# Kernel optimization log

Hardware: AMD Instinct MI355X
Metric: run time of the kernel (lower is better)

Reference implementation:

```python
import jax, jax.numpy as jnp
import numpy as np

ALPHA = 0.2  # LeakyReLU negative slope
NEG = -1e12


def setup_inputs() -> dict:
    key = jax.random.key(0)
    ks = jax.random.split(key, 7)
    B, N, Cin, F, H = 4, 2048, 256, 64, 4
    x = jax.random.normal(ks[0], (B, N, Cin), dtype=jnp.float32)
    adj = jax.random.randint(ks[1], (N, N), 0, 2, dtype=jnp.int32)
    W = jax.random.normal(ks[2], (H, Cin, F), dtype=jnp.float32) * (1.414 / np.sqrt(Cin))
    a1 = jax.random.normal(ks[3], (H, F), dtype=jnp.float32) * 0.1
    a2 = jax.random.normal(ks[4], (H, F), dtype=jnp.float32) * 0.1
    Wl = jax.random.normal(ks[5], (F, H * F), dtype=jnp.float32) * (1.0 / np.sqrt(H * F))
    bl = jax.random.normal(ks[6], (F,), dtype=jnp.float32) * 0.01
    return {"x": x, "adj": adj, "W": W, "a1": a1, "a2": a2, "Wl": Wl, "bl": bl}


def leaky(v):
    return jnp.where(v >= 0, v, ALPHA * v)


def reference(x, adj, W, a1, a2, Wl, bl):
    # Eval mode: dropout is a no-op.
    # h: [B,H,N,F] per-head projected features
    h = jnp.einsum("bnc,hcf->bhnf", x, W)
    # additive attention: e[b,h,i,j] = leaky(h_i . a1 + h_j . a2)
    f1 = jnp.einsum("bhnf,hf->bhn", h, a1)  # source term
    f2 = jnp.einsum("bhnf,hf->bhn", h, a2)  # target term
    e = leaky(f1[:, :, :, None] + f2[:, :, None, :])  # [B,H,N,N]
    e = jnp.where(adj[None, None] > 0, e, NEG)
    # NOTE: original softmaxes over dim=1 of [B,N,N], i.e. the i axis (axis=2 here)
    att = jax.nn.softmax(e, axis=2)
    hp = jnp.einsum("bhij,bhjf->bhif", att, h)  # [B,H,N,F]
    hp = jax.nn.relu(hp)  # concat=True heads
    B, H, N, F = hp.shape
    cat = hp.transpose(0, 2, 1, 3).reshape(B, N, H * F)
    out = leaky(cat @ Wl.T + bl)  # n_heads > 1 -> linear + leakyrelu
    return out
```

## Files before the change

### kernel.cpp

```cpp
#include <hip/hip_runtime.h>
#include <hip/hip_bf16.h>
#include <stdint.h>

typedef __attribute__((ext_vector_type(8))) short short8;
typedef __attribute__((ext_vector_type(4))) float f32x4;
typedef uint32_t u32;
typedef uint16_t u16;
typedef uint8_t u8;

#define LOG2E 1.4426950408889634f


__device__ __forceinline__ u16 f2bf(float f){
  union{float f; u32 u;} x; x.f = f;
  u32 r = x.u + 0x7FFFu + ((x.u >> 16) & 1u);
  return (u16)(r >> 16);
}
__device__ __forceinline__ u32 pkbf(float a, float b){
  __hip_bfloat162 h = __float22bfloat162_rn(float2{a, b});
  union{ __hip_bfloat162 h; u32 u; } cv; cv.h = h;
  return cv.u;
}
__device__ __forceinline__ float bflo(u32 cd){ union{u32 u; float f;} v; v.u = cd << 16; return v.f; }
__device__ __forceinline__ float bfhi(u32 cd){ union{u32 u; float f;} v; v.u = cd & 0xFFFF0000u; return v.f; }

__global__ __launch_bounds__(256) void k_front(const float* __restrict__ x,
      const float* __restrict__ W, const float* __restrict__ a1, const float* __restrict__ a2,
      const int* __restrict__ adj,
      u8* __restrict__ adjb, u16* __restrict__ hT,
      float* __restrict__ Aarr, float* __restrict__ Barr,
      float* __restrict__ Cexp, float* __restrict__ Dexp){
  int bid = blockIdx.x, t = threadIdx.x;

  if (bid >= 512){
    int idx = (bid - 512)*256 + t;
    const int4* ap = (const int4*)(adj + (size_t)idx*8);
    int4 v0 = ap[0], v1 = ap[1];
    u32 byte = (u32)(v0.x > 0)        | ((u32)(v0.y > 0) << 1)
             | ((u32)(v0.z > 0) << 2) | ((u32)(v0.w > 0) << 3)
             | ((u32)(v1.x > 0) << 4) | ((u32)(v1.y > 0) << 5)
             | ((u32)(v1.z > 0) << 6) | ((u32)(v1.w > 0) << 7);
    adjb[idx] = (u8)byte;
    return;
  }
  __shared__ u16 WL[64*264];
  int rt = bid & 127, cb = bid >> 7;
  const float* Wh = W + (size_t)cb*16384;
  #pragma unroll 4
  for (int p = 0; p < 16; p++){
    int idx = p*256 + t;
    float4 wv = ((const float4*)Wh)[idx];
    int off = idx*4; int c = off >> 6, f0 = off & 63;
    int cc = c ^ (((f0 >> 2) & 7) << 3);
    WL[(f0+0)*264 + cc] = f2bf(wv.x);
    WL[(f0+1)*264 + cc] = f2bf(wv.y);
    WL[(f0+2)*264 + cc] = f2bf(wv.z);
    WL[(f0+3)*264 + cc] = f2bf(wv.w);
  }
  __syncthreads();

  int w = t >> 6, l = t & 63;
  int rA = rt*64 + w*16 + (l & 15);
  int kg = (l >> 4) * 8;
  int rowq[4], rswq[4];
  #pragma unroll
  for (int q = 0; q < 4; q++){
    rowq[q] = q*16 + (l & 15);
    rswq[q] = ((rowq[q] >> 2) & 7) << 3;
  }
  f32x4 acc[4] = {};
  const float* xrow = x + (size_t)rA * 256;
  #pragma unroll
  for (int ks = 0; ks < 8; ks++){
    int c = ks*32 + kg;
    float4 xa = *(const float4*)(xrow + c);
    float4 xb = *(const float4*)(xrow + c + 4);
    union{u32 w[4]; short8 v;} A;
    A.w[0] = pkbf(xa.x, xa.y); A.w[1] = pkbf(xa.z, xa.w);
    A.w[2] = pkbf(xb.x, xb.y); A.w[3] = pkbf(xb.z, xb.w);
    #pragma unroll
    for (int q = 0; q < 4; q++){
      short8 Bf = *(const short8*)&WL[rowq[q]*264 + (c ^ rswq[q])];
      acc[q] = __builtin_amdgcn_mfma_f32_16x16x32_bf16(A.v, Bf, acc[q], 0, 0, 0);
    }
  }
  int rb = rt*64 + w*16 + (l >> 4)*4;
  int b = rb >> 11, n = rb & 2047;
  #pragma unroll
  for (int q = 0; q < 4; q++){
    int f = q*16 + (l & 15);
    u32 p0 = pkbf(acc[q][0], acc[q][1]);
    u32 p1 = pkbf(acc[q][2], acc[q][3]);
    u16* dst = hT + ((size_t)(b*4 + cb)*64 + f)*2048 + n;
    *(uint2*)dst = uint2{p0, p1};
  }
  float a1v[4], a2v[4];
  #pragma unroll
  for (int q = 0; q < 4; q++){
    a1v[q] = a1[cb*64 + q*16 + (l & 15)];
    a2v[q] = a2[cb*64 + q*16 + (l & 15)];
  }
  float s1[4], s2[4];
  #pragma unroll
  for (int r = 0; r < 4; r++){
    s1[r] = acc[0][r]*a1v[0] + acc[1][r]*a1v[1] + acc[2][r]*a1v[2] + acc[3][r]*a1v[3];
    s2[r] = acc[0][r]*a2v[0] + acc[1][r]*a2v[1] + acc[2][r]*a2v[2] + acc[3][r]*a2v[3];
  }
  #pragma unroll
  for (int m = 1; m <= 8; m <<= 1){
    #pragma unroll
    for (int r = 0; r < 4; r++){
      s1[r] += __shfl_xor(s1[r], m);
      s2[r] += __shfl_xor(s2[r], m);
    }
  }
  if ((l & 15) == 0){
    #pragma unroll
    for (int r = 0; r < 4; r++){
      int row = rb + r;
      int bb = row >> 11, nn = row & 2047;
      int o = (bb*4 + cb)*2048 + nn;
      float fa = s1[r] * LOG2E;
      Aarr[o] = __builtin_amdgcn_exp2f(fa);
      Barr[o] = __builtin_amdgcn_exp2f(0.2f*fa);
      float fb = s2[r] * LOG2E;
      Cexp[o] = __builtin_amdgcn_exp2f(fb);
      Dexp[o] = __builtin_amdgcn_exp2f(0.2f*fb);
    }
  }
}

__global__ __launch_bounds__(256) void k_colsum(const u32* __restrict__ adjw,
      const float* __restrict__ Aarr, const float* __restrict__ Barr,
      const float* __restrict__ Cexp, const float* __restrict__ Dexp,
      float* __restrict__ partial){
  __shared__ float AL[128*16], BL[128*16];
  __shared__ float red[4][1024];
  int jt = blockIdx.x;
  int is = blockIdx.y;
  int t = threadIdx.x, w = t >> 6, l = t & 63;
  int i0 = is*128;
  for (int k = t; k < 2048; k += 256){
    int bh = k >> 7, ii = k & 127;
    float av = Aarr[bh*2048 + i0 + ii];
    float bv = Barr[bh*2048 + i0 + ii];
    AL[ii*16 + bh] = av;
    BL[ii*16 + bh] = bv;
  }
  int j = jt*64 + l;
  float Cj[16], Dj[16];
  #pragma unroll
  for (int bh = 0; bh < 16; bh++){
    Cj[bh] = Cexp[bh*2048 + j];
    Dj[bh] = Dexp[bh*2048 + j];
  }
  float acc[16] = {};
  __syncthreads();
  int wi = jt*2 + (l >> 5), sh = l & 31;
  const u32* aw = adjw + wi;
  #pragma unroll 2
  for (int ii = w*32; ii < w*32 + 32; ii++){
    u32 m = aw[(size_t)(i0 + ii)*64];
    float bitf = (float)((m >> sh) & 1u);
    const float* ar = &AL[ii*16];
    const float* br = &BL[ii*16];
    #pragma unroll
    for (int q = 0; q < 4; q++){
      float4 a4 = *(const float4*)(ar + q*4);
      float4 b4 = *(const float4*)(br + q*4);
      acc[q*4+0] = fmaf(fmaxf(a4.x*Cj[q*4+0], b4.x*Dj[q*4+0]), bitf, acc[q*4+0]);
      acc[q*4+1] = fmaf(fmaxf(a4.y*Cj[q*4+1], b4.y*Dj[q*4+1]), bitf, acc[q*4+1]);
      acc[q*4+2] = fmaf(fmaxf(a4.z*Cj[q*4+2], b4.z*Dj[q*4+2]), bitf, acc[q*4+2]);
      acc[q*4+3] = fmaf(fmaxf(a4.w*Cj[q*4+3], b4.w*Dj[q*4+3]), bitf, acc[q*4+3]);
    }
  }
  #pragma unroll
  for (int bh = 0; bh < 16; bh++) red[w][bh*64 + l] = acc[bh];
  __syncthreads();
  #pragma unroll
  for (int k = 0; k < 4; k++){
    int e = t*4 + k;
    float s = (red[0][e] + red[1][e]) + (red[2][e] + red[3][e]);
    int bh = e >> 6, jl = e & 63;
    partial[((size_t)is*16 + bh)*2048 + jt*64 + jl] = s;
  }
}

__global__ __launch_bounds__(256) void k_cd(const float* __restrict__ partial,
      const float* __restrict__ Cexp, const float* __restrict__ Dexp,
      u32* __restrict__ CD){
  int t = blockIdx.x*256 + threadIdx.x;
  float s = 0.f;
  #pragma unroll
  for (int is = 0; is < 16; is++) s += partial[(size_t)is*32768 + t];
  float inv = 1.0f / s;
  CD[t] = pkbf(Cexp[t]*inv, Dexp[t]*inv);
}

__global__ __launch_bounds__(256) void k_pv(const u32* __restrict__ adjw, const u16* __restrict__ hT,
      const float* __restrict__ Aarr, const float* __restrict__ Barr,
      const u32* __restrict__ CD, float* __restrict__ part){
  int it = blockIdx.x;
  int bh = blockIdx.y;
  int jh = blockIdx.z;
  int b = bh >> 2, h = bh & 3;
  int t = threadIdx.x;
  int w = t >> 6, l = t & 63;

  __shared__ u16 hTl[64*136];

  int i0 = it*128 + w*32 + (l & 15);
  float Ai0 = Aarr[bh*2048 + i0],      Bi0 = Barr[bh*2048 + i0];
  float Ai1 = Aarr[bh*2048 + i0 + 16], Bi1 = Barr[bh*2048 + i0 + 16];
  const u32* CDr = CD + bh*2048;
  const u16* hTr = hT + (size_t)bh * 64 * 2048;
  int kg = (l >> 4) * 8;
  f32x4 acc[2][4] = {};

  for (int jj = 0; jj < 1024; jj += 128){
    int jc = jh*1024 + jj;
    __syncthreads();
    {
      int f = t >> 2, seg = (t & 3) * 32;
      const u16* src = hTr + (size_t)f*2048 + jc + seg;
      u16* d = hTl + f*136 + seg;
      *(uint4*)(d)      = *(const uint4*)(src);
      *(uint4*)(d + 8)  = *(const uint4*)(src + 8);
      *(uint4*)(d + 16) = *(const uint4*)(src + 16);
      *(uint4*)(d + 24) = *(const uint4*)(src + 24);
    }
    __syncthreads();
    uint4 mw0 = *(const uint4*)(adjw + (size_t)i0*64 + (jc >> 5));
    uint4 mw1 = *(const uint4*)(adjw + (size_t)(i0+16)*64 + (jc >> 5));
    #pragma unroll
    for (int ks = 0; ks < 4; ks++){
      u32 cd[8];
      *(uint4*)(cd)     = *(const uint4*)(CDr + jc + ks*32 + kg);
      *(uint4*)(cd + 4) = *(const uint4*)(CDr + jc + ks*32 + kg + 4);
      u32 w0 = (&mw0.x)[ks] >> kg;
      u32 w1 = (&mw1.x)[ks] >> kg;
      float wv0[8], wv1[8];
      #pragma unroll
      for (int e = 0; e < 8; e++){
        float ca = bflo(cd[e]), db = bfhi(cd[e]);
        float ev0 = fmaxf(Ai0*ca, Bi0*db);
        float ev1 = fmaxf(Ai1*ca, Bi1*db);
        wv0[e] = ((int)(w0 << (31-e)) < 0) ? ev0 : 0.f;
        wv1[e] = ((int)(w1 << (31-e)) < 0) ? ev1 : 0.f;
      }
      union{u32 w[4]; short8 v;} A0, A1;
      A0.w[0] = pkbf(wv0[0], wv0[1]); A0.w[1] = pkbf(wv0[2], wv0[3]);
      A0.w[2] = pkbf(wv0[4], wv0[5]); A0.w[3] = pkbf(wv0[6], wv0[7]);
      A1.w[0] = pkbf(wv1[0], wv1[1]); A1.w[1] = pkbf(wv1[2], wv1[3]);
      A1.w[2] = pkbf(wv1[4], wv1[5]); A1.w[3] = pkbf(wv1[6], wv1[7]);
      #pragma unroll
      for (int q = 0; q < 4; q++){
        short8 Bf = *(const short8*)&hTl[(q*16 + (l & 15))*136 + ks*32 + kg];
        acc[0][q] = __builtin_amdgcn_mfma_f32_16x16x32_bf16(A0.v, Bf, acc[0][q], 0, 0, 0);
        acc[1][q] = __builtin_amdgcn_mfma_f32_16x16x32_bf16(A1.v, Bf, acc[1][q], 0, 0, 0);
      }
    }
  }
  float* pr = part + ((size_t)(jh*4 + b)*2048)*256;
  #pragma unroll
  for (int r = 0; r < 2; r++){
    int nb = it*128 + w*32 + r*16 + (l >> 4)*4;
    #pragma unroll
    for (int q = 0; q < 4; q++){
      int f = h*64 + q*16 + (l & 15);
      #pragma unroll
      for (int rr = 0; rr < 4; rr++){
        pr[(size_t)(nb + rr)*256 + f] = acc[r][q][rr];
      }
    }
  }
}

__global__ __launch_bounds__(256) void k_out(const float* __restrict__ part,
                       const float* __restrict__ Wl, const float* __restrict__ bl,
                       float* __restrict__ out){
  int rt = blockIdx.x;
  int w = threadIdx.x >> 6, l = threadIdx.x & 63;
  int rA = rt*64 + w*16 + (l & 15);
  int b = rA >> 11, n = rA & 2047;
  const float* p0 = part + ((size_t)b*2048 + n)*256;
  const float* p1 = part + ((size_t)(4 + b)*2048 + n)*256;
  int kg = (l >> 4) * 8;
  f32x4 acc[4] = {};
  #pragma unroll
  for (int ks = 0; ks < 8; ks++){
    int c = ks*32 + kg;
    float4 x0 = *(const float4*)(p0 + c);
    float4 x1 = *(const float4*)(p0 + c + 4);
    float4 y0 = *(const float4*)(p1 + c);
    float4 y1 = *(const float4*)(p1 + c + 4);
    float av[8];
    av[0] = fmaxf(x0.x + y0.x, 0.f); av[1] = fmaxf(x0.y + y0.y, 0.f);
    av[2] = fmaxf(x0.z + y0.z, 0.f); av[3] = fmaxf(x0.w + y0.w, 0.f);
    av[4] = fmaxf(x1.x + y1.x, 0.f); av[5] = fmaxf(x1.y + y1.y, 0.f);
    av[6] = fmaxf(x1.z + y1.z, 0.f); av[7] = fmaxf(x1.w + y1.w, 0.f);
    union{u32 w[4]; short8 v;} A;
    A.w[0] = pkbf(av[0], av[1]); A.w[1] = pkbf(av[2], av[3]);
    A.w[2] = pkbf(av[4], av[5]); A.w[3] = pkbf(av[6], av[7]);
    #pragma unroll
    for (int q = 0; q < 4; q++){
      const float* wr = Wl + (size_t)(q*16 + (l & 15))*256 + c;
      float4 u0 = *(const float4*)(wr);
      float4 u1 = *(const float4*)(wr + 4);
      union{u32 w[4]; short8 v;} Bv;
      Bv.w[0] = pkbf(u0.x, u0.y); Bv.w[1] = pkbf(u0.z, u0.w);
      Bv.w[2] = pkbf(u1.x, u1.y); Bv.w[3] = pkbf(u1.z, u1.w);
      acc[q] = __builtin_amdgcn_mfma_f32_16x16x32_bf16(A.v, Bv.v, acc[q], 0, 0, 0);
    }
  }
  int rb = rt*64 + w*16 + (l >> 4)*4;
  #pragma unroll
  for (int q = 0; q < 4; q++){
    int o = q*16 + (l & 15);
    float bv = bl[o];
    #pragma unroll
    for (int r = 0; r < 4; r++){
      float v = acc[q][r] + bv;
      out[(size_t)(rb + r)*64 + o] = fmaxf(v, 0.2f*v);
    }
  }
}

extern "C" void kernel_launch(void* const* d_in, const int* in_sizes, int n_in,
                              void* d_out, int out_size, void* d_ws, size_t ws_size,
                              hipStream_t stream) {
  const float* x  = (const float*)d_in[0];
  const int* adj  = (const int*)d_in[1];
  const float* W  = (const float*)d_in[2];
  const float* a1 = (const float*)d_in[3];
  const float* a2 = (const float*)d_in[4];
  const float* Wl = (const float*)d_in[5];
  const float* bl = (const float*)d_in[6];
  float* out = (float*)d_out;
  char* ws = (char*)d_ws;

  u32* adjw    = (u32*)(ws + 0x0000000);
  u16* hT      = (u16*)(ws + 0x0080000);
  float* part  = (float*)(ws + 0x0480000);
  float* Aarr  = (float*)(ws + 0x1480000);
  float* Barr  = (float*)(ws + 0x14A0000);
  float* Cexp  = (float*)(ws + 0x14C0000);
  float* Dexp  = (float*)(ws + 0x14E0000);
  u32* CD      = (u32*)(ws + 0x1500000);

  k_front<<<2560, 256, 0, stream>>>(x, W, a1, a2, adj, (u8*)adjw, hT, Aarr, Barr, Cexp, Dexp);
  k_colsum<<<dim3(32, 16), 256, 0, stream>>>(adjw, Aarr, Barr, Cexp, Dexp, part);
  k_cd<<<128, 256, 0, stream>>>(part, Cexp, Dexp, CD);
  k_pv<<<dim3(16, 16, 2), 256, 0, stream>>>(adjw, hT, Aarr, Barr, CD, part);
  k_out<<<128, 256, 0, stream>>>(part, Wl, bl, out);
}
```

Baseline: 77.66 us.

## Remove k_cd kernel: atomic column sums and fold normalization into k_pv

The column sums in k_colsum are now accumulated with float atomicAdd into a Dsum buffer, which extra blocks in k_front zero first. The separate k_cd reduction kernel is removed. Each k_pv block computes the normalized bf16 C/D pairs for its 1024-column half into shared memory and reads them from LDS instead of global memory. This saves one kernel launch and one partial-buffer round trip, at the cost of atomic contention, nondeterministic summation order, and recomputing the reciprocal in every k_pv block.

```diff
diff --git a/kernel.cpp b/kernel.cpp
--- a/kernel.cpp
+++ b/kernel.cpp
@@ -29,9 +29,14 @@
       const int* __restrict__ adj,
       u8* __restrict__ adjb, u16* __restrict__ hT,
       float* __restrict__ Aarr, float* __restrict__ Barr,
-      float* __restrict__ Cexp, float* __restrict__ Dexp){
+      float* __restrict__ Cexp, float* __restrict__ Dexp,
+      float* __restrict__ Dsum){
   int bid = blockIdx.x, t = threadIdx.x;
 
+  if (bid >= 2560){
+    Dsum[(bid - 2560)*256 + t] = 0.f;
+    return;
+  }
   if (bid >= 512){
     int idx = (bid - 512)*256 + t;
     const int4* ap = (const int4*)(adj + (size_t)idx*8);
@@ -133,7 +138,7 @@
 __global__ __launch_bounds__(256) void k_colsum(const u32* __restrict__ adjw,
       const float* __restrict__ Aarr, const float* __restrict__ Barr,
       const float* __restrict__ Cexp, const float* __restrict__ Dexp,
-      float* __restrict__ partial){
+      float* __restrict__ Dsum){
   __shared__ float AL[128*16], BL[128*16];
   __shared__ float red[4][1024];
   int jt = blockIdx.x;
@@ -142,10 +147,8 @@
   int i0 = is*128;
   for (int k = t; k < 2048; k += 256){
     int bh = k >> 7, ii = k & 127;
-    float av = Aarr[bh*2048 + i0 + ii];
-    float bv = Barr[bh*2048 + i0 + ii];
-    AL[ii*16 + bh] = av;
-    BL[ii*16 + bh] = bv;
+    AL[ii*16 + bh] = Aarr[bh*2048 + i0 + ii];
+    BL[ii*16 + bh] = Barr[bh*2048 + i0 + ii];
   }
   int j = jt*64 + l;
   float Cj[16], Dj[16];
@@ -182,24 +185,14 @@
     int e = t*4 + k;
     float s = (red[0][e] + red[1][e]) + (red[2][e] + red[3][e]);
     int bh = e >> 6, jl = e & 63;
-    partial[((size_t)is*16 + bh)*2048 + jt*64 + jl] = s;
-  }
-}
-
-__global__ __launch_bounds__(256) void k_cd(const float* __restrict__ partial,
-      const float* __restrict__ Cexp, const float* __restrict__ Dexp,
-      u32* __restrict__ CD){
-  int t = blockIdx.x*256 + threadIdx.x;
-  float s = 0.f;
-  #pragma unroll
-  for (int is = 0; is < 16; is++) s += partial[(size_t)is*32768 + t];
-  float inv = 1.0f / s;
-  CD[t] = pkbf(Cexp[t]*inv, Dexp[t]*inv);
+    atomicAdd(&Dsum[bh*2048 + jt*64 + jl], s);
+  }
 }
 
 __global__ __launch_bounds__(256) void k_pv(const u32* __restrict__ adjw, const u16* __restrict__ hT,
       const float* __restrict__ Aarr, const float* __restrict__ Barr,
-      const u32* __restrict__ CD, float* __restrict__ part){
+      const float* __restrict__ Cexp, const float* __restrict__ Dexp,
+      const float* __restrict__ Dsum, float* __restrict__ part){
   int it = blockIdx.x;
   int bh = blockIdx.y;
   int jh = blockIdx.z;
@@ -208,11 +201,25 @@
   int w = t >> 6, l = t & 63;
 
   __shared__ u16 hTl[64*136];
+  __shared__ u32 CDl[1024];
+
+  {
+    int gj = bh*2048 + jh*1024 + t*4;
+    float4 c4 = *(const float4*)(Cexp + gj);
+    float4 d4 = *(const float4*)(Dexp + gj);
+    float4 s4 = *(const float4*)(Dsum + gj);
+    float i0v = 1.0f/s4.x, i1v = 1.0f/s4.y, i2v = 1.0f/s4.z, i3v = 1.0f/s4.w;
+    uint4 pk;
+    pk.x = pkbf(c4.x*i0v, d4.x*i0v);
+    pk.y = pkbf(c4.y*i1v, d4.y*i1v);
+    pk.z = pkbf(c4.z*i2v, d4.z*i2v);
+    pk.w = pkbf(c4.w*i3v, d4.w*i3v);
+    *(uint4*)&CDl[t*4] = pk;
+  }
 
   int i0 = it*128 + w*32 + (l & 15);
   float Ai0 = Aarr[bh*2048 + i0],      Bi0 = Barr[bh*2048 + i0];
   float Ai1 = Aarr[bh*2048 + i0 + 16], Bi1 = Barr[bh*2048 + i0 + 16];
-  const u32* CDr = CD + bh*2048;
   const u16* hTr = hT + (size_t)bh * 64 * 2048;
   int kg = (l >> 4) * 8;
   f32x4 acc[2][4] = {};
@@ -235,8 +242,8 @@
     #pragma unroll
     for (int ks = 0; ks < 4; ks++){
       u32 cd[8];
-      *(uint4*)(cd)     = *(const uint4*)(CDr + jc + ks*32 + kg);
-      *(uint4*)(cd + 4) = *(const uint4*)(CDr + jc + ks*32 + kg + 4);
+      *(uint4*)(cd)     = *(const uint4*)&CDl[jj + ks*32 + kg];
+      *(uint4*)(cd + 4) = *(const uint4*)&CDl[jj + ks*32 + kg + 4];
       u32 w0 = (&mw0.x)[ks] >> kg;
       u32 w1 = (&mw1.x)[ks] >> kg;
       float wv0[8], wv1[8];
@@ -346,11 +353,10 @@
   float* Barr  = (float*)(ws + 0x14A0000);
   float* Cexp  = (float*)(ws + 0x14C0000);
   float* Dexp  = (float*)(ws + 0x14E0000);
-  u32* CD      = (u32*)(ws + 0x1500000);
-
-  k_front<<<2560, 256, 0, stream>>>(x, W, a1, a2, adj, (u8*)adjw, hT, Aarr, Barr, Cexp, Dexp);
-  k_colsum<<<dim3(32, 16), 256, 0, stream>>>(adjw, Aarr, Barr, Cexp, Dexp, part);
-  k_cd<<<128, 256, 0, stream>>>(part, Cexp, Dexp, CD);
-  k_pv<<<dim3(16, 16, 2), 256, 0, stream>>>(adjw, hT, Aarr, Barr, CD, part);
+  float* Dsum  = (float*)(ws + 0x1500000);
+
+  k_front<<<2688, 256, 0, stream>>>(x, W, a1, a2, adj, (u8*)adjw, hT, Aarr, Barr, Cexp, Dexp, Dsum);
+  k_colsum<<<dim3(32, 16), 256, 0, stream>>>(adjw, Aarr, Barr, Cexp, Dexp, Dsum);
+  k_pv<<<dim3(16, 16, 2), 256, 0, stream>>>(adjw, hT, Aarr, Barr, Cexp, Dexp, Dsum, part);
   k_out<<<128, 256, 0, stream>>>(part, Wl, bl, out);
 }
```

New measurement: 73.26 us. 1.06x faster.
